# Performance work log

Measured on AMD Instinct MI355X. Metric: run time of the kernel, lower is better.

The kernel has to match this reference:

```python
import jax, jax.numpy as jnp
import numpy as np

N_USER = 80000
N_ITEM = 20000
N = N_USER + N_ITEM          # total nodes
E = 1600000                  # edges (nnz of norm_adj), avg degree 16
EMB = 64                     # emb_size
FEAT = 64                    # feature_dim -> input_dim = 128
D = EMB + FEAT               # 128
L = 3                        # number of GCN layers, layer_size=[128,128,128]
K = 3                        # max_hop
B = 4096                     # batch_size


def setup_inputs() -> dict:
    key = jax.random.key(0)
    ks = jax.random.split(key, 16)
    deg_scale = 1.0 / 16.0  # ~normalized adjacency values
    return {
        'edge_row': jax.random.randint(ks[0], (E,), 0, N, dtype=jnp.int32),
        'edge_col': jax.random.randint(ks[1], (E,), 0, N, dtype=jnp.int32),
        'edge_val': jax.random.uniform(ks[2], (E,), dtype=jnp.float32) * deg_scale,
        'feat': jax.random.normal(ks[3], (N_USER, FEAT), dtype=jnp.float32) * 0.1,
        'user_emb': jax.random.normal(ks[4], (N_USER, EMB), dtype=jnp.float32) * 0.1,
        'item_emb1': jax.random.normal(ks[5], (N_ITEM, EMB), dtype=jnp.float32) * 0.1,
        'item_emb2': jax.random.normal(ks[6], (N_ITEM, FEAT), dtype=jnp.float32) * 0.1,
        'alphas': jax.random.normal(ks[7], (L, K), dtype=jnp.float32) * 0.1,
        'W_gc': jax.random.normal(ks[8], (L, D, D), dtype=jnp.float32) * 0.05,
        'b_gc': jax.random.normal(ks[9], (L, 1, D), dtype=jnp.float32) * 0.05,
        'W_bi': jax.random.normal(ks[10], (L, D, D), dtype=jnp.float32) * 0.05,
        'b_bi': jax.random.normal(ks[11], (L, 1, D), dtype=jnp.float32) * 0.05,
        'users': jax.random.randint(ks[12], (B,), 0, N_USER, dtype=jnp.int32),
        'pos_items': jax.random.randint(ks[13], (B,), 0, N_ITEM, dtype=jnp.int32),
        'neg_items': jax.random.randint(ks[14], (B,), 0, N_ITEM, dtype=jnp.int32),
    }


def reference(edge_row, edge_col, edge_val, feat, user_emb, item_emb1,
              item_emb2, alphas, W_gc, b_gc, W_bi, b_bi,
              users, pos_items, neg_items):
    def spmm(X):
        # A_hat @ X via edge-list gather + segment-sum (sparse.mm equivalent)
        return jax.ops.segment_sum(edge_val[:, None] * X[edge_col], edge_row,
                                   num_segments=N)

    # ego embeddings: [[user_emb|feat], [item_emb1|item_emb2]] -> [N, D]
    ego = jnp.concatenate([
        jnp.concatenate([user_emb, item_emb1], axis=0),
        jnp.concatenate([feat, item_emb2], axis=0),
    ], axis=1)

    all_embs = [ego]
    for k in range(L):
        # multi-order aggregation: sum_i beta_i * A^i @ ego
        beta = jax.nn.softmax(alphas[k])
        cur = spmm(ego)
        side = beta[0] * cur
        for i in range(1, K):
            cur = spmm(cur)
            side = side + beta[i] * cur
        sum_e = side @ W_gc[k] + b_gc[k]
        bi_e = (ego * side) @ W_bi[k] + b_bi[k]
        # aggregator_mode == 'sum_bi'
        ego = jax.nn.leaky_relu(sum_e, negative_slope=0.2) + bi_e
        # mess_dropout = 0 -> identity; L2-normalize rows (F.normalize eps=1e-12)
        norm = ego / jnp.maximum(
            jnp.linalg.norm(ego, axis=1, keepdims=True), 1e-12)
        all_embs.append(norm)

    all_emb = jnp.concatenate(all_embs, axis=1)  # [N, D*(L+1)] = [N, 512]
    u_emb = all_emb[:N_USER]
    i_emb = all_emb[N_USER:]
    return (u_emb[users], i_emb[pos_items], i_emb[neg_items])
```

## Files before the change

kernel.cpp:

```cpp
#include <hip/hip_runtime.h>
#include <hip/hip_bf16.h>

typedef __hip_bfloat16 hbf16;
typedef unsigned short u16;
typedef __bf16 bf16x8 __attribute__((ext_vector_type(8)));
typedef float f32x4 __attribute__((ext_vector_type(4)));

#define N_USERS 80000
#define N_ITEMS 20000
#define NTOT    100000
#define NEDGE   1600000
#define DDIM    128
#define NLAY    3
#define KHOP    3
#define NB      4096
#define LBM     128
#define NBUK    49
#define BROWS   2048

__device__ inline u16 f2bfu(float f) { __bf16 h = (__bf16)f; return __builtin_bit_cast(u16, h); }

__global__ void beta_kernel(const float* __restrict__ alphas, float* __restrict__ beta) {
    if (threadIdx.x == 0 && blockIdx.x == 0) {
        for (int k = 0; k < NLAY; ++k) {
            float a[KHOP];
            float m = -1e30f;
            for (int i = 0; i < KHOP; ++i) { a[i] = alphas[k*KHOP+i]; m = fmaxf(m, a[i]); }
            float s = 0.f;
            for (int i = 0; i < KHOP; ++i) { a[i] = expf(a[i] - m); s += a[i]; }
            for (int i = 0; i < KHOP; ++i) beta[k*KHOP+i] = a[i] / s;
        }
    }
}

__global__ void build_ego_kernel(const float* __restrict__ feat, const float* __restrict__ user_emb,
                                 const float* __restrict__ item_emb1, const float* __restrict__ item_emb2,
                                 u16* __restrict__ ego) {
    int i = blockIdx.x * 256 + threadIdx.x;
    int n = i >> 7, d = i & 127;
    float v;
    if (n < N_USERS) {
        v = (d < 64) ? user_emb[n*64 + d] : feat[n*64 + d - 64];
    } else {
        int m = n - N_USERS;
        v = (d < 64) ? item_emb1[m*64 + d] : item_emb2[m*64 + d - 64];
    }
    ego[i] = f2bfu(v);
}

__global__ void transpose_w_kernel(const float* __restrict__ Wgc, const float* __restrict__ Wbi,
                                   u16* __restrict__ WTgc, u16* __restrict__ WTbi) {
    __shared__ float t[32][33];
    int z = blockIdx.z;
    const float* W = (z < 3) ? (Wgc + (size_t)z * 16384) : (Wbi + (size_t)(z - 3) * 16384);
    u16* WT = (z < 3) ? (WTgc + (size_t)z * 16384) : (WTbi + (size_t)(z - 3) * 16384);
    int r0 = blockIdx.y * 32, c0 = blockIdx.x * 32;
    for (int i = threadIdx.y; i < 32; i += 8)
        t[i][threadIdx.x] = W[(size_t)(r0 + i) * 128 + c0 + threadIdx.x];
    __syncthreads();
    for (int i = threadIdx.y; i < 32; i += 8)
        WT[(size_t)(c0 + i) * 128 + r0 + threadIdx.x] = f2bfu(t[threadIdx.x][i]);
}

__global__ void zero_kernel(int* __restrict__ p, int n) {
    int i = blockIdx.x * 256 + threadIdx.x;
    if (i < n) p[i] = 0;
}

__global__ __launch_bounds__(256) void bhist_kernel(const int* __restrict__ er,
                                                    int* __restrict__ bbins) {
    __shared__ int l[NBUK];
    int tid = threadIdx.x;
    if (tid < NBUK) l[tid] = 0;
    __syncthreads();
    for (int i = blockIdx.x * 256 + tid; i < NEDGE; i += gridDim.x * 256)
        atomicAdd(&l[er[i] >> 11], 1);
    __syncthreads();
    if (tid < NBUK && l[tid]) atomicAdd(&bbins[tid], l[tid]);
}

__global__ void bscan_kernel(const int* __restrict__ bbins, int* __restrict__ bbase,
                             int* __restrict__ bcur) {
    if (threadIdx.x == 0 && blockIdx.x == 0) {
        int acc = 0;
        for (int b = 0; b < NBUK; ++b) { int t = bbins[b]; bbase[b] = acc; bcur[b] = acc; acc += t; }
        bbase[NBUK] = acc;
    }
}

__global__ __launch_bounds__(256) void bappend_kernel(
    const int* __restrict__ er, const int* __restrict__ ec, const float* __restrict__ ev,
    int* __restrict__ bcur, int* __restrict__ tmprow, int2* __restrict__ tmpcv) {
    __shared__ int lcnt[NBUK], lbase[NBUK], lrank[NBUK];
    int tid = threadIdx.x;
    for (int b = tid; b < NBUK; b += 256) { lcnt[b] = 0; lrank[b] = 0; }
    __syncthreads();
    int base = blockIdx.x * 2048;
    int r[8], c[8], vb[8], bk[8];
    bool ok[8];
    #pragma unroll
    for (int k = 0; k < 8; ++k) {
        int i = base + k * 256 + tid;
        ok[k] = i < NEDGE;
        bk[k] = 0;
        if (ok[k]) {
            r[k] = er[i]; c[k] = ec[i]; vb[k] = __float_as_int(ev[i]);
            bk[k] = r[k] >> 11;
            atomicAdd(&lcnt[bk[k]], 1);
        }
    }
    __syncthreads();
    for (int b = tid; b < NBUK; b += 256)
        lbase[b] = lcnt[b] ? atomicAdd(&bcur[b], lcnt[b]) : 0;
    __syncthreads();
    #pragma unroll
    for (int k = 0; k < 8; ++k) {
        if (ok[k]) {
            int rank = atomicAdd(&lrank[bk[k]], 1);
            int pos = lbase[bk[k]] + rank;
            tmprow[pos] = r[k];
            tmpcv[pos] = make_int2(c[k], vb[k]);
        }
    }
}

__global__ __launch_bounds__(1024) void bfinal_kernel(
    const int* __restrict__ bbase, const int* __restrict__ tmprow,
    const int2* __restrict__ tmpcv, int* __restrict__ rowptr, int2* __restrict__ edges) {
    __shared__ int lhist[BROWS];
    __shared__ int lbase[BROWS];
    __shared__ int s2[1024];
    int b = blockIdx.x, tid = threadIdx.x;
    int s = bbase[b], e = bbase[b + 1];
    int rbase = b << 11;
    int nrows = min(NTOT - rbase, BROWS);
    lhist[tid] = 0; lhist[tid + 1024] = 0;
    __syncthreads();
    for (int i = s + tid; i < e; i += 1024)
        atomicAdd(&lhist[tmprow[i] - rbase], 1);
    __syncthreads();
    int a0 = lhist[tid * 2], a1 = lhist[tid * 2 + 1];
    s2[tid] = a0 + a1;
    __syncthreads();
    for (int off = 1; off < 1024; off <<= 1) {
        int t = (tid >= off) ? s2[tid - off] : 0;
        __syncthreads();
        s2[tid] += t;
        __syncthreads();
    }
    int excl = s2[tid] - a0 - a1;
    lbase[tid * 2] = excl;
    lbase[tid * 2 + 1] = excl + a0;
    __syncthreads();
    for (int j = tid; j < nrows; j += 1024)
        rowptr[rbase + j] = s + lbase[j];
    if (b == NBUK - 1 && tid == 0) rowptr[NTOT] = NEDGE;
    lhist[tid * 2] = lbase[tid * 2];
    lhist[tid * 2 + 1] = lbase[tid * 2 + 1];
    __syncthreads();
    for (int i = s + tid; i < e; i += 1024) {
        int lr = tmprow[i] - rbase;
        int p = atomicAdd(&lhist[lr], 1);
        edges[s + p] = tmpcv[i];
    }
}

__device__ inline void ld_edge_nt(const int2* __restrict__ p, int& c, float& v) {
    unsigned long long rec =
        __builtin_nontemporal_load(reinterpret_cast<const unsigned long long*>(p));
    c = (int)(unsigned)(rec & 0xffffffffull);
    v = __int_as_float((int)(unsigned)(rec >> 32));
}

__global__ __launch_bounds__(256) void spmm_kernel(
    const int* __restrict__ rowptr, const int2* __restrict__ edges,
    const u16* __restrict__ X, u16* __restrict__ Y) {
    int tid = threadIdx.x;
    int r = blockIdx.x * 16 + (tid >> 4);
    int lane = tid & 15;
    int s = rowptr[r], e = rowptr[r + 1];
    float acc[8];
    #pragma unroll
    for (int i = 0; i < 8; ++i) acc[i] = 0.f;
    const u16* xb = X + lane * 8;
    int j = s;
    for (; j + 8 <= e; j += 8) {
        int cc[8]; float vv[8];
        #pragma unroll
        for (int u = 0; u < 8; ++u) ld_edge_nt(edges + j + u, cc[u], vv[u]);
        bf16x8 x[8];
        #pragma unroll
        for (int u = 0; u < 8; ++u)
            x[u] = *reinterpret_cast<const bf16x8*>(xb + (size_t)cc[u] * DDIM);
        __builtin_amdgcn_sched_barrier(0);
        #pragma unroll
        for (int u = 0; u < 8; ++u) {
            #pragma unroll
            for (int i = 0; i < 8; ++i) acc[i] = fmaf(vv[u], (float)x[u][i], acc[i]);
        }
    }
    for (; j + 4 <= e; j += 4) {
        int cc[4]; float vv[4];
        #pragma unroll
        for (int u = 0; u < 4; ++u) ld_edge_nt(edges + j + u, cc[u], vv[u]);
        bf16x8 x[4];
        #pragma unroll
        for (int u = 0; u < 4; ++u)
            x[u] = *reinterpret_cast<const bf16x8*>(xb + (size_t)cc[u] * DDIM);
        __builtin_amdgcn_sched_barrier(0);
        #pragma unroll
        for (int u = 0; u < 4; ++u) {
            #pragma unroll
            for (int i = 0; i < 8; ++i) acc[i] = fmaf(vv[u], (float)x[u][i], acc[i]);
        }
    }
    for (; j < e; ++j) {
        int cc; float vv;
        ld_edge_nt(edges + j, cc, vv);
        bf16x8 x = *reinterpret_cast<const bf16x8*>(xb + (size_t)cc * DDIM);
        #pragma unroll
        for (int i = 0; i < 8; ++i) acc[i] = fmaf(vv, (float)x[i], acc[i]);
    }
    size_t oi = (size_t)r * DDIM + lane * 8;
    bf16x8 y;
    #pragma unroll
    for (int i = 0; i < 8; ++i) y[i] = (__bf16)acc[i];
    *reinterpret_cast<bf16x8*>(Y + oi) = y;
}

__global__ __launch_bounds__(512, 4) void layer_kernel(
    const u16* __restrict__ ego, const u16* __restrict__ h1,
    const u16* __restrict__ h2, const u16* __restrict__ h3,
    const float* __restrict__ beta3,
    const u16* __restrict__ wtgc, const u16* __restrict__ wtbi,
    const float* __restrict__ bgc, const float* __restrict__ bbi,
    u16* __restrict__ ego_out, u16* __restrict__ normbuf) {
    __shared__ __align__(16) unsigned char smem[65536];
    const int WG = 0, WB = 32768;
    int tid = threadIdx.x;
    int base = blockIdx.x * LBM;
    float b0 = beta3[0], b1 = beta3[1], b2 = beta3[2];

    #pragma unroll
    for (int p = 0; p < 4; ++p) {
        int slot = tid + p * 512;
        int n = slot >> 4, ks = slot & 15;
        uint4 g  = *reinterpret_cast<const uint4*>(wtgc + n * DDIM + ks * 8);
        uint4 bq = *reinterpret_cast<const uint4*>(wtbi + n * DDIM + ks * 8);
        int addr = n * 256 + ((ks * 16) ^ ((n & 7) << 4));
        *reinterpret_cast<uint4*>(&smem[WG + addr]) = g;
        *reinterpret_cast<uint4*>(&smem[WB + addr]) = bq;
    }
    __syncthreads();

    int l = tid & 63, w = tid >> 6;
    int m = l & 15, g16 = l >> 4;
    int sw = (m & 7) << 4;
    int grow = base + w * 16 + m;
    bool ok = grow < NTOT;
    int grc = ok ? grow : 0;
    size_t aoff = (size_t)grc * DDIM + g16 * 8;

    f32x4 accg[8], accb[8];
    #pragma unroll
    for (int nt = 0; nt < 8; ++nt) {
        accg[nt] = (f32x4){0.f, 0.f, 0.f, 0.f};
        accb[nt] = (f32x4){0.f, 0.f, 0.f, 0.f};
    }
    #pragma unroll
    for (int kk = 0; kk < 4; ++kk) {
        bf16x8 x1 = *reinterpret_cast<const bf16x8*>(h1 + aoff + kk * 32);
        bf16x8 x2 = *reinterpret_cast<const bf16x8*>(h2 + aoff + kk * 32);
        bf16x8 x3 = *reinterpret_cast<const bf16x8*>(h3 + aoff + kk * 32);
        bf16x8 ev = *reinterpret_cast<const bf16x8*>(ego + aoff + kk * 32);
        bf16x8 as, ab;
        #pragma unroll
        for (int i = 0; i < 8; ++i) {
            float sf = ok ? (b0 * (float)x1[i] + b1 * (float)x2[i] + b2 * (float)x3[i]) : 0.f;
            as[i] = (__bf16)sf;
            ab[i] = (__bf16)(sf * (float)ev[i]);
        }
        int ka = (kk * 64 + g16 * 16) ^ sw;
        #pragma unroll
        for (int nt = 0; nt < 8; ++nt) {
            int na = (nt * 16 + m) * 256 + ka;
            bf16x8 bg = *reinterpret_cast<const bf16x8*>(&smem[WG + na]);
            accg[nt] = __builtin_amdgcn_mfma_f32_16x16x32_bf16(as, bg, accg[nt], 0, 0, 0);
            bf16x8 bb = *reinterpret_cast<const bf16x8*>(&smem[WB + na]);
            accb[nt] = __builtin_amdgcn_mfma_f32_16x16x32_bf16(ab, bb, accb[nt], 0, 0, 0);
        }
    }
    float bgv[8], bbv[8];
    #pragma unroll
    for (int nt = 0; nt < 8; ++nt) { bgv[nt] = bgc[nt * 16 + m]; bbv[nt] = bbi[nt * 16 + m]; }
    float vv[8][4];
    float ss[4] = {0.f, 0.f, 0.f, 0.f};
    #pragma unroll
    for (int nt = 0; nt < 8; ++nt) {
        #pragma unroll
        for (int rr = 0; rr < 4; ++rr) {
            float se = accg[nt][rr] + bgv[nt];
            float be = accb[nt][rr] + bbv[nt];
            float v = (se > 0.f ? se : 0.2f * se) + be;
            vv[nt][rr] = v;
            ss[rr] += v * v;
            int row = base + w * 16 + g16 * 4 + rr;
            if (row < NTOT) ego_out[(size_t)row * DDIM + nt * 16 + m] = f2bfu(v);
        }
    }
    #pragma unroll
    for (int rr = 0; rr < 4; ++rr) {
        ss[rr] += __shfl_xor(ss[rr], 1, 64);
        ss[rr] += __shfl_xor(ss[rr], 2, 64);
        ss[rr] += __shfl_xor(ss[rr], 4, 64);
        ss[rr] += __shfl_xor(ss[rr], 8, 64);
        ss[rr] = 1.f / fmaxf(sqrtf(ss[rr]), 1e-12f);
    }
    #pragma unroll
    for (int nt = 0; nt < 8; ++nt) {
        #pragma unroll
        for (int rr = 0; rr < 4; ++rr) {
            int row = base + w * 16 + g16 * 4 + rr;
            if (row < NTOT) normbuf[(size_t)row * DDIM + nt * 16 + m] = f2bfu(vv[nt][rr] * ss[rr]);
        }
    }
}

__global__ void gather_ego_kernel(const float* __restrict__ feat, const float* __restrict__ user_emb,
                                  const float* __restrict__ item_emb1, const float* __restrict__ item_emb2,
                                  const int* __restrict__ users, const int* __restrict__ pos,
                                  const int* __restrict__ neg, float* __restrict__ out) {
    int i = blockIdx.x * 256 + threadIdx.x;
    int which = i / (NB * DDIM);
    int rem = i - which * (NB * DDIM);
    int b = rem >> 7, d = rem & 127;
    float v;
    if (which == 0) {
        int u = users[b];
        v = (d < 64) ? user_emb[u*64 + d] : feat[u*64 + d - 64];
    } else {
        int m = (which == 1) ? pos[b] : neg[b];
        v = (d < 64) ? item_emb1[m*64 + d] : item_emb2[m*64 + d - 64];
    }
    out[(size_t)which * NB * 512 + (size_t)b * 512 + d] = v;
}

__global__ void gather_slice_kernel(const u16* __restrict__ src, const int* __restrict__ users,
                                    const int* __restrict__ pos, const int* __restrict__ neg,
                                    float* __restrict__ out, int slot) {
    int i = blockIdx.x * 256 + threadIdx.x;
    int which = i / (NB * DDIM);
    int rem = i - which * (NB * DDIM);
    int b = rem >> 7, c = rem & 127;
    int row;
    if (which == 0)      row = users[b];
    else if (which == 1) row = N_USERS + pos[b];
    else                 row = N_USERS + neg[b];
    unsigned int u = src[(size_t)row * DDIM + c];
    out[(size_t)which * NB * 512 + (size_t)b * 512 + slot * 128 + c] =
        __builtin_bit_cast(float, u << 16);
}

extern "C" void kernel_launch(void* const* d_in, const int* in_sizes, int n_in,
                              void* d_out, int out_size, void* d_ws, size_t ws_size,
                              hipStream_t stream) {
    (void)in_sizes; (void)n_in; (void)out_size; (void)ws_size;
    const int*   edge_row  = (const int*)  d_in[0];
    const int*   edge_col  = (const int*)  d_in[1];
    const float* edge_val  = (const float*)d_in[2];
    const float* feat      = (const float*)d_in[3];
    const float* user_emb  = (const float*)d_in[4];
    const float* item_emb1 = (const float*)d_in[5];
    const float* item_emb2 = (const float*)d_in[6];
    const float* alphas    = (const float*)d_in[7];
    const float* W_gc      = (const float*)d_in[8];
    const float* b_gc      = (const float*)d_in[9];
    const float* W_bi      = (const float*)d_in[10];
    const float* b_bi      = (const float*)d_in[11];
    const int*   users     = (const int*)  d_in[12];
    const int*   pos_items = (const int*)  d_in[13];
    const int*   neg_items = (const int*)  d_in[14];
    float* out = (float*)d_out;

    char* ws = (char*)d_ws;
    size_t off = 0;
    auto alloc = [&](size_t bytes) -> char* {
        char* p = ws + off;
        off = (off + bytes + 255) & ~(size_t)255;
        return p;
    };
    u16*   ego      = (u16*)  alloc((size_t)NTOT * DDIM * 2);
    u16*   h1       = (u16*)  alloc((size_t)NTOT * DDIM * 2);
    u16*   h2       = (u16*)  alloc((size_t)NTOT * DDIM * 2);
    u16*   h3       = (u16*)  alloc((size_t)NTOT * DDIM * 2);
    u16*   normbuf  = (u16*)  alloc((size_t)NTOT * DDIM * 2);
    int*   rowptr   = (int*)  alloc((size_t)(NTOT + 1) * 4);
    int*   bbins    = (int*)  alloc((NBUK + 2) * 4);
    int*   bbase    = (int*)  alloc((NBUK + 2) * 4);
    int*   bcur     = (int*)  alloc((NBUK + 2) * 4);
    int2*  edges    = (int2*) alloc((size_t)NEDGE * 8);
    u16*   wtgc     = (u16*)  alloc((size_t)NLAY * DDIM * DDIM * 2);
    u16*   wtbi     = (u16*)  alloc((size_t)NLAY * DDIM * DDIM * 2);
    float* beta     = (float*)alloc(256);

    int*  tmprow = (int*)h1;
    int2* tmpcv  = (int2*)((char*)h1 + (size_t)NEDGE * 4);

    beta_kernel<<<1, 64, 0, stream>>>(alphas, beta);
    build_ego_kernel<<<(NTOT * DDIM) / 256, 256, 0, stream>>>(feat, user_emb, item_emb1, item_emb2, ego);
    transpose_w_kernel<<<dim3(4, 4, 6), dim3(32, 8), 0, stream>>>(W_gc, W_bi, wtgc, wtbi);

    zero_kernel<<<1, 64, 0, stream>>>(bbins, NBUK);
    bhist_kernel<<<512, 256, 0, stream>>>(edge_row, bbins);
    bscan_kernel<<<1, 64, 0, stream>>>(bbins, bbase, bcur);
    bappend_kernel<<<(NEDGE + 2047) / 2048, 256, 0, stream>>>(edge_row, edge_col, edge_val,
                                                              bcur, tmprow, tmpcv);
    bfinal_kernel<<<NBUK, 1024, 0, stream>>>(bbase, tmprow, tmpcv, rowptr, edges);

    gather_ego_kernel<<<(3 * NB * DDIM) / 256, 256, 0, stream>>>(feat, user_emb, item_emb1, item_emb2,
                                                                 users, pos_items, neg_items, out);

    int lgrid = (NTOT + LBM - 1) / LBM;
    for (int k = 0; k < NLAY; ++k) {
        spmm_kernel<<<NTOT / 16, 256, 0, stream>>>(rowptr, edges, ego, h1);
        spmm_kernel<<<NTOT / 16, 256, 0, stream>>>(rowptr, edges, h1, h2);
        spmm_kernel<<<NTOT / 16, 256, 0, stream>>>(rowptr, edges, h2, h3);
        layer_kernel<<<lgrid, 512, 0, stream>>>(ego, h1, h2, h3, beta + 3 * k,
                                                wtgc + (size_t)k * DDIM * DDIM, wtbi + (size_t)k * DDIM * DDIM,
                                                b_gc + (size_t)k * DDIM, b_bi + (size_t)k * DDIM,
                                                ego, normbuf);
        gather_slice_kernel<<<(3 * NB * DDIM) / 256, 256, 0, stream>>>(normbuf, users, pos_items, neg_items, out, k + 1);
    }
}
```

Baseline: 853.6 us.

## Merge small setup kernels, double bucket count, prefetch layer operands

Folds the beta softmax into the bucket-scan kernel and the bucket-bin zeroing into build_ego, which removes two tiny kernel launches. The row bucket count is doubled (1024 rows per bucket) so bfinal runs 98 blocks with a simpler one-element-per-thread scan, and bhist now uses half as many blocks. In layer_kernel the next k-slice of h1/h2/h3/ego is loaded one iteration ahead to hide global load latency behind the MFMAs, and the accumulator registers are reused for the output values. The prefetch raises register pressure, and zeroing bbins inside build_ego depends on stream ordering before bhist runs.

```diff
diff --git a/kernel.cpp b/kernel.cpp
--- a/kernel.cpp
+++ b/kernel.cpp
@@ -15,27 +15,16 @@
 #define KHOP    3
 #define NB      4096
 #define LBM     128
-#define NBUK    49
-#define BROWS   2048
+#define NBUK    98
+#define BROWS   1024
+#define BSH     10
 
 __device__ inline u16 f2bfu(float f) { __bf16 h = (__bf16)f; return __builtin_bit_cast(u16, h); }
-
-__global__ void beta_kernel(const float* __restrict__ alphas, float* __restrict__ beta) {
-    if (threadIdx.x == 0 && blockIdx.x == 0) {
-        for (int k = 0; k < NLAY; ++k) {
-            float a[KHOP];
-            float m = -1e30f;
-            for (int i = 0; i < KHOP; ++i) { a[i] = alphas[k*KHOP+i]; m = fmaxf(m, a[i]); }
-            float s = 0.f;
-            for (int i = 0; i < KHOP; ++i) { a[i] = expf(a[i] - m); s += a[i]; }
-            for (int i = 0; i < KHOP; ++i) beta[k*KHOP+i] = a[i] / s;
-        }
-    }
-}
 
 __global__ void build_ego_kernel(const float* __restrict__ feat, const float* __restrict__ user_emb,
                                  const float* __restrict__ item_emb1, const float* __restrict__ item_emb2,
-                                 u16* __restrict__ ego) {
+                                 u16* __restrict__ ego, int* __restrict__ bbins) {
+    if (blockIdx.x == 0 && threadIdx.x < NBUK) bbins[threadIdx.x] = 0;
     int i = blockIdx.x * 256 + threadIdx.x;
     int n = i >> 7, d = i & 127;
     float v;
@@ -62,11 +51,6 @@
         WT[(size_t)(c0 + i) * 128 + r0 + threadIdx.x] = f2bfu(t[threadIdx.x][i]);
 }
 
-__global__ void zero_kernel(int* __restrict__ p, int n) {
-    int i = blockIdx.x * 256 + threadIdx.x;
-    if (i < n) p[i] = 0;
-}
-
 __global__ __launch_bounds__(256) void bhist_kernel(const int* __restrict__ er,
                                                     int* __restrict__ bbins) {
     __shared__ int l[NBUK];
@@ -74,14 +58,23 @@
     if (tid < NBUK) l[tid] = 0;
     __syncthreads();
     for (int i = blockIdx.x * 256 + tid; i < NEDGE; i += gridDim.x * 256)
-        atomicAdd(&l[er[i] >> 11], 1);
+        atomicAdd(&l[er[i] >> BSH], 1);
     __syncthreads();
     if (tid < NBUK && l[tid]) atomicAdd(&bbins[tid], l[tid]);
 }
 
-__global__ void bscan_kernel(const int* __restrict__ bbins, int* __restrict__ bbase,
-                             int* __restrict__ bcur) {
+__global__ void beta_bscan_kernel(const float* __restrict__ alphas, float* __restrict__ beta,
+                                  const int* __restrict__ bbins, int* __restrict__ bbase,
+                                  int* __restrict__ bcur) {
     if (threadIdx.x == 0 && blockIdx.x == 0) {
+        for (int k = 0; k < NLAY; ++k) {
+            float a[KHOP];
+            float m = -1e30f;
+            for (int i = 0; i < KHOP; ++i) { a[i] = alphas[k*KHOP+i]; m = fmaxf(m, a[i]); }
+            float s = 0.f;
+            for (int i = 0; i < KHOP; ++i) { a[i] = expf(a[i] - m); s += a[i]; }
+            for (int i = 0; i < KHOP; ++i) beta[k*KHOP+i] = a[i] / s;
+        }
         int acc = 0;
         for (int b = 0; b < NBUK; ++b) { int t = bbins[b]; bbase[b] = acc; bcur[b] = acc; acc += t; }
         bbase[NBUK] = acc;
@@ -105,7 +98,7 @@
         bk[k] = 0;
         if (ok[k]) {
             r[k] = er[i]; c[k] = ec[i]; vb[k] = __float_as_int(ev[i]);
-            bk[k] = r[k] >> 11;
+            bk[k] = r[k] >> BSH;
             atomicAdd(&lcnt[bk[k]], 1);
         }
     }
@@ -128,19 +121,18 @@
     const int* __restrict__ bbase, const int* __restrict__ tmprow,
     const int2* __restrict__ tmpcv, int* __restrict__ rowptr, int2* __restrict__ edges) {
     __shared__ int lhist[BROWS];
-    __shared__ int lbase[BROWS];
     __shared__ int s2[1024];
     int b = blockIdx.x, tid = threadIdx.x;
     int s = bbase[b], e = bbase[b + 1];
-    int rbase = b << 11;
+    int rbase = b << BSH;
     int nrows = min(NTOT - rbase, BROWS);
-    lhist[tid] = 0; lhist[tid + 1024] = 0;
+    lhist[tid] = 0;
     __syncthreads();
     for (int i = s + tid; i < e; i += 1024)
         atomicAdd(&lhist[tmprow[i] - rbase], 1);
     __syncthreads();
-    int a0 = lhist[tid * 2], a1 = lhist[tid * 2 + 1];
-    s2[tid] = a0 + a1;
+    int a = lhist[tid];
+    s2[tid] = a;
     __syncthreads();
     for (int off = 1; off < 1024; off <<= 1) {
         int t = (tid >= off) ? s2[tid - off] : 0;
@@ -148,15 +140,10 @@
         s2[tid] += t;
         __syncthreads();
     }
-    int excl = s2[tid] - a0 - a1;
-    lbase[tid * 2] = excl;
-    lbase[tid * 2 + 1] = excl + a0;
-    __syncthreads();
-    for (int j = tid; j < nrows; j += 1024)
-        rowptr[rbase + j] = s + lbase[j];
+    int excl = s2[tid] - a;
+    if (tid < nrows) rowptr[rbase + tid] = s + excl;
     if (b == NBUK - 1 && tid == 0) rowptr[NTOT] = NEDGE;
-    lhist[tid * 2] = lbase[tid * 2];
-    lhist[tid * 2 + 1] = lbase[tid * 2 + 1];
+    lhist[tid] = excl;
     __syncthreads();
     for (int i = s + tid; i < e; i += 1024) {
         int lr = tmprow[i] - rbase;
@@ -261,6 +248,11 @@
     int grc = ok ? grow : 0;
     size_t aoff = (size_t)grc * DDIM + g16 * 8;
 
+    bf16x8 c1 = *reinterpret_cast<const bf16x8*>(h1 + aoff);
+    bf16x8 c2 = *reinterpret_cast<const bf16x8*>(h2 + aoff);
+    bf16x8 c3 = *reinterpret_cast<const bf16x8*>(h3 + aoff);
+    bf16x8 ce = *reinterpret_cast<const bf16x8*>(ego + aoff);
+
     f32x4 accg[8], accb[8];
     #pragma unroll
     for (int nt = 0; nt < 8; ++nt) {
@@ -269,16 +261,20 @@
     }
     #pragma unroll
     for (int kk = 0; kk < 4; ++kk) {
-        bf16x8 x1 = *reinterpret_cast<const bf16x8*>(h1 + aoff + kk * 32);
-        bf16x8 x2 = *reinterpret_cast<const bf16x8*>(h2 + aoff + kk * 32);
-        bf16x8 x3 = *reinterpret_cast<const bf16x8*>(h3 + aoff + kk * 32);
-        bf16x8 ev = *reinterpret_cast<const bf16x8*>(ego + aoff + kk * 32);
+        bf16x8 p1, p2, p3, pe;
+        if (kk < 3) {
+            p1 = *reinterpret_cast<const bf16x8*>(h1 + aoff + (kk + 1) * 32);
+            p2 = *reinterpret_cast<const bf16x8*>(h2 + aoff + (kk + 1) * 32);
+            p3 = *reinterpret_cast<const bf16x8*>(h3 + aoff + (kk + 1) * 32);
+            pe = *reinterpret_cast<const bf16x8*>(ego + aoff + (kk + 1) * 32);
+            __builtin_amdgcn_sched_barrier(0);
+        }
         bf16x8 as, ab;
         #pragma unroll
         for (int i = 0; i < 8; ++i) {
-            float sf = ok ? (b0 * (float)x1[i] + b1 * (float)x2[i] + b2 * (float)x3[i]) : 0.f;
+            float sf = ok ? (b0 * (float)c1[i] + b1 * (float)c2[i] + b2 * (float)c3[i]) : 0.f;
             as[i] = (__bf16)sf;
-            ab[i] = (__bf16)(sf * (float)ev[i]);
+            ab[i] = (__bf16)(sf * (float)ce[i]);
         }
         int ka = (kk * 64 + g16 * 16) ^ sw;
         #pragma unroll
@@ -289,11 +285,11 @@
             bf16x8 bb = *reinterpret_cast<const bf16x8*>(&smem[WB + na]);
             accb[nt] = __builtin_amdgcn_mfma_f32_16x16x32_bf16(ab, bb, accb[nt], 0, 0, 0);
         }
+        if (kk < 3) { c1 = p1; c2 = p2; c3 = p3; ce = pe; }
     }
     float bgv[8], bbv[8];
     #pragma unroll
     for (int nt = 0; nt < 8; ++nt) { bgv[nt] = bgc[nt * 16 + m]; bbv[nt] = bbi[nt * 16 + m]; }
-    float vv[8][4];
     float ss[4] = {0.f, 0.f, 0.f, 0.f};
     #pragma unroll
     for (int nt = 0; nt < 8; ++nt) {
@@ -302,7 +298,7 @@
             float se = accg[nt][rr] + bgv[nt];
             float be = accb[nt][rr] + bbv[nt];
             float v = (se > 0.f ? se : 0.2f * se) + be;
-            vv[nt][rr] = v;
+            accg[nt][rr] = v;
             ss[rr] += v * v;
             int row = base + w * 16 + g16 * 4 + rr;
             if (row < NTOT) ego_out[(size_t)row * DDIM + nt * 16 + m] = f2bfu(v);
@@ -321,7 +317,7 @@
         #pragma unroll
         for (int rr = 0; rr < 4; ++rr) {
             int row = base + w * 16 + g16 * 4 + rr;
-            if (row < NTOT) normbuf[(size_t)row * DDIM + nt * 16 + m] = f2bfu(vv[nt][rr] * ss[rr]);
+            if (row < NTOT) normbuf[(size_t)row * DDIM + nt * 16 + m] = f2bfu(accg[nt][rr] * ss[rr]);
         }
     }
 }
@@ -406,13 +402,12 @@
     int*  tmprow = (int*)h1;
     int2* tmpcv  = (int2*)((char*)h1 + (size_t)NEDGE * 4);
 
-    beta_kernel<<<1, 64, 0, stream>>>(alphas, beta);
-    build_ego_kernel<<<(NTOT * DDIM) / 256, 256, 0, stream>>>(feat, user_emb, item_emb1, item_emb2, ego);
+    build_ego_kernel<<<(NTOT * DDIM) / 256, 256, 0, stream>>>(feat, user_emb, item_emb1, item_emb2,
+                                                              ego, bbins);
     transpose_w_kernel<<<dim3(4, 4, 6), dim3(32, 8), 0, stream>>>(W_gc, W_bi, wtgc, wtbi);
 
-    zero_kernel<<<1, 64, 0, stream>>>(bbins, NBUK);
-    bhist_kernel<<<512, 256, 0, stream>>>(edge_row, bbins);
-    bscan_kernel<<<1, 64, 0, stream>>>(bbins, bbase, bcur);
+    bhist_kernel<<<256, 256, 0, stream>>>(edge_row, bbins);
+    beta_bscan_kernel<<<1, 64, 0, stream>>>(alphas, beta, bbins, bbase, bcur);
     bappend_kernel<<<(NEDGE + 2047) / 2048, 256, 0, stream>>>(edge_row, edge_col, edge_val,
                                                               bcur, tmprow, tmpcv);
     bfinal_kernel<<<NBUK, 1024, 0, stream>>>(bbase, tmprow, tmpcv, rowptr, edges);
```

Result: faster. 801.9 us (-6.0%).
